# Performance work log

Measured on AMD Instinct MI355X. Metric: run time of the kernel, lower is better.

Reference implementation:

```python
import jax, jax.numpy as jnp
import numpy as np
from jax import lax

A_NUM = 2
N_LAYER = 4
DIM0 = 64   # fr_inner_dim_0 == signal_dim_0 (forced by view/squeeze logic)
DIM1 = 256  # fr_inner_dim_1
SD0 = 64
SD1 = 64
K_OUT = 8
UPS = 4
EPS = 1e-5
BSZ = 64


def setup_inputs() -> dict:
    key = jax.random.key(0)
    ks = jax.random.split(key, 16)
    s = 0.05
    f32 = jnp.float32
    inp = jax.random.normal(ks[0], (BSZ, 2, SD0, SD1), f32)
    # ComplexConv2d2 weights stored squeezed to their effective matmul form.
    W_in_r = jax.random.normal(ks[1], (DIM1 * A_NUM, SD1), f32) * s
    W_in_i = jax.random.normal(ks[2], (DIM1 * A_NUM, SD1), f32) * s
    W_pre_r = jax.random.normal(ks[3], (A_NUM,), f32) * s
    W_pre_i = jax.random.normal(ks[4], (A_NUM,), f32) * s
    Wm_r = jax.random.normal(ks[5], (2 * N_LAYER, SD0, SD0), f32) * s
    Wm_i = jax.random.normal(ks[6], (2 * N_LAYER, SD0, SD0), f32) * s
    Wc_r = jax.random.normal(ks[7], (N_LAYER, A_NUM), f32) * s
    Wc_i = jax.random.normal(ks[8], (N_LAYER, A_NUM), f32) * s
    W_l3_r = jax.random.normal(ks[9], (DIM0 * A_NUM, SD0), f32) * s
    W_l3_i = jax.random.normal(ks[10], (DIM0 * A_NUM, SD0), f32) * s
    conv1_w = jax.random.normal(ks[11], (N_LAYER, A_NUM, A_NUM, 3, 3), f32) * s
    conv2_w = jax.random.normal(ks[12], (N_LAYER, A_NUM, A_NUM, 3, 3), f32) * s
    bn1_g = jnp.ones((N_LAYER, A_NUM), f32)
    bn1_b = jnp.zeros((N_LAYER, A_NUM), f32)
    bn2_g = jnp.ones((N_LAYER, A_NUM), f32)
    bn2_b = jnp.zeros((N_LAYER, A_NUM), f32)
    W_out = jax.random.normal(ks[13], (A_NUM, 1, K_OUT, K_OUT), f32) * s
    return {"inp": inp, "W_in_r": W_in_r, "W_in_i": W_in_i, "W_pre_r": W_pre_r,
            "W_pre_i": W_pre_i, "Wm_r": Wm_r, "Wm_i": Wm_i, "Wc_r": Wc_r,
            "Wc_i": Wc_i, "W_l3_r": W_l3_r, "W_l3_i": W_l3_i,
            "conv1_w": conv1_w, "bn1_g": bn1_g, "bn1_b": bn1_b,
            "conv2_w": conv2_w, "bn2_g": bn2_g, "bn2_b": bn2_b, "W_out": W_out}


def _circ_conv(x, w):
    xp = jnp.pad(x, ((0, 0), (0, 0), (1, 1), (1, 1)), mode='wrap')
    return lax.conv_general_dilated(xp, w, (1, 1), 'VALID',
                                    dimension_numbers=('NCHW', 'OIHW', 'NCHW'))


def _bn(x, g, b):
    mu = jnp.mean(x, axis=(0, 2, 3), keepdims=True)
    var = jnp.var(x, axis=(0, 2, 3), keepdims=True)
    return (x - mu) * lax.rsqrt(var + EPS) * g[None, :, None, None] + b[None, :, None, None]


def _forward(inp, W_in_r, W_in_i, W_pre_r, W_pre_i, Wm_r, Wm_i, Wc_r, Wc_i,
             W_l3_r, W_l3_i, conv1_w, bn1_g, bn1_b, conv2_w, bn2_g, bn2_b, W_out):
    bsz = inp.shape[0]
    xr, xi = inp[:, 0], inp[:, 1]  # (b, sd0, sd1)
    # input_layer: complex conv, kernel (1, sd1) -> contraction over width
    yr = jnp.einsum('bhw,cw->bch', xr, W_in_r) - jnp.einsum('bhw,cw->bch', xi, W_in_i)
    yi = jnp.einsum('bhw,cw->bch', xi, W_in_r) + jnp.einsum('bhw,cw->bch', xr, W_in_i)
    xreal = yr.reshape(bsz, A_NUM, DIM1, DIM0).transpose(0, 1, 3, 2)  # (b,A,dim0,dim1)
    ximag = yi.reshape(bsz, A_NUM, DIM1, DIM0).transpose(0, 1, 3, 2)
    # concat_pre: complex 1x1 conv, A_NUM -> 1 channel
    x_real = (jnp.einsum('bahw,a->bhw', xreal, W_pre_r) - jnp.einsum('bahw,a->bhw', ximag, W_pre_i))[:, None]
    x_imag = (jnp.einsum('bahw,a->bhw', ximag, W_pre_r) + jnp.einsum('bahw,a->bhw', xreal, W_pre_i))[:, None]
    Gr, Gi = x_real, x_imag  # loop-invariant Gnk

    def phase_branch(xr_, xi_, Wr, Wi):
        a, c = xr_[:, 0], xi_[:, 0]  # (b, dim0, dim1)
        # complex conv kernel (sd0,1) == matmul over height
        Ir = (jnp.einsum('bhw,ch->bcw', a, Wr) - jnp.einsum('bhw,ch->bcw', c, Wi))[:, None]
        Ii = (jnp.einsum('bhw,ch->bcw', c, Wr) + jnp.einsum('bhw,ch->bcw', a, Wi))[:, None]
        s_ = 1.0 + jnp.log(Ir * Ir + Ii * Ii)
        EIr, EIi = s_ * Ir, -s_ * Ii
        ur, ui = Wr.T, Wi.T
        zr = jnp.einsum('hc,bncw->bnhw', ur, EIr) - jnp.einsum('hc,bncw->bnhw', ui, EIi)
        zi = jnp.einsum('hc,bncw->bnhw', ur, EIi) + jnp.einsum('hc,bncw->bnhw', ui, EIr)
        wr = jnp.sum(Gr * zr - Gi * zi, axis=3)  # (b,1,dim0)
        wi = jnp.sum(Gr * zi + Gi * zr, axis=3)
        ang = jnp.arctan2(wi, wr)[..., None]  # broadcast over dim1
        cr, ci = jnp.cos(ang), -jnp.sin(ang)
        return Gr * cr - Gi * ci, Gr * ci + Gi * cr

    for i in range(N_LAYER):
        x1r, x1i = phase_branch(x_real, x_imag, Wm_r[i], Wm_i[i])
        x2r, x2i = phase_branch(x_real, x_imag, Wm_r[i + N_LAYER], Wm_i[i + N_LAYER])
        sr = jnp.concatenate([x1r, x2r], 1)
        si = jnp.concatenate([x1i, x2i], 1)
        x_real = (jnp.einsum('bahw,a->bhw', sr, Wc_r[i]) - jnp.einsum('bahw,a->bhw', si, Wc_i[i]))[:, None]
        x_imag = (jnp.einsum('bahw,a->bhw', si, Wc_r[i]) + jnp.einsum('bahw,a->bhw', sr, Wc_i[i]))[:, None]

    # input_layer3: complex conv kernel (sd0,1), 1 -> dim0*A_NUM channels
    a, c = x_real[:, 0], x_imag[:, 0]
    fr = (jnp.einsum('bhw,ch->bcw', a, W_l3_r) - jnp.einsum('bhw,ch->bcw', c, W_l3_i)).reshape(bsz, -1)
    fi = (jnp.einsum('bhw,ch->bcw', c, W_l3_r) + jnp.einsum('bhw,ch->bcw', a, W_l3_i)).reshape(bsz, -1)
    m = jnp.max(jnp.sqrt(fr * fr + fi * fi), axis=1, keepdims=True)
    fr, fi = fr / m, fi / m
    fr = fr.reshape(bsz, A_NUM, DIM0, DIM1)
    fi = fi.reshape(bsz, A_NUM, DIM0, DIM1)
    x = jnp.sqrt(fr * fr + fi * fi)

    for i in range(N_LAYER):
        h = jax.nn.relu(_bn(_circ_conv(x, conv1_w[i]), bn1_g[i], bn1_b[i]))
        h = _bn(_circ_conv(h, conv2_w[i]), bn2_g[i], bn2_b[i])
        x = jax.nn.relu(x + h)

    # ConvTranspose2d(A_NUM, 1, K_OUT, stride=UPS, padding=2, output_padding=1)
    wt = jnp.flip(W_out, (2, 3)).transpose(1, 0, 2, 3)  # (1, A_NUM, k, k)
    pad_lo = K_OUT - 1 - 2
    pad_hi = pad_lo + 1
    y = lax.conv_general_dilated(x, wt, (1, 1),
                                 [(pad_lo, pad_hi), (pad_lo, pad_hi)],
                                 lhs_dilation=(UPS, UPS),
                                 dimension_numbers=('NCHW', 'OIHW', 'NCHW'))
    return y[:, 0]


def reference(inp, W_in_r, W_in_i, W_pre_r, W_pre_i, Wm_r, Wm_i, Wc_r, Wc_i,
              W_l3_r, W_l3_i, conv1_w, bn1_g, bn1_b, conv2_w, bn2_g, bn2_b, W_out):
    return _forward(inp, W_in_r, W_in_i, W_pre_r, W_pre_i, Wm_r, Wm_i, Wc_r, Wc_i,
                    W_l3_r, W_l3_i, conv1_w, bn1_g, bn1_b, conv2_w, bn2_g, bn2_b, W_out)
```

## Files before the change

### kernel.cpp

```cpp
#include <hip/hip_runtime.h>
#include <hip/hip_bf16.h>
#include <math.h>


__global__ void k0_prep(const float* __restrict__ Wr, const float* __restrict__ Wi,
                        const float* __restrict__ pr, const float* __restrict__ pi,
                        float* __restrict__ ArT, float* __restrict__ AiT,
                        float2* __restrict__ C) {
    int w  = blockIdx.x;
    int w2 = threadIdx.x;
    float p0r = pr[0], p1r = pr[1], p0i = pi[0], p1i = pi[1];
    float wr0 = Wr[w2 * 64 + w],         wi0 = Wi[w2 * 64 + w];
    float wr1 = Wr[(256 + w2) * 64 + w], wi1 = Wi[(256 + w2) * 64 + w];
    ArT[w * 256 + w2] = p0r * wr0 - p0i * wi0 + p1r * wr1 - p1i * wi1;
    AiT[w * 256 + w2] = p0r * wi0 + p0i * wr0 + p1r * wi1 + p1i * wr1;
    if (w2 < 64) C[w * 64 + w2] = make_float2(1.f, 0.f);
}

__global__ __launch_bounds__(256) void k1_G(const float* __restrict__ inp,
                                            const float* __restrict__ ArT,
                                            const float* __restrict__ AiT,
                                            float* __restrict__ Gr, float* __restrict__ Gi) {
    int hc = blockIdx.x;
    int b  = blockIdx.y;
    int t  = threadIdx.x;
    __shared__ float sxr[8][64], sxi[8][64];
    int base_r = (b * 2 + 0) * 4096 + hc * 8 * 64;
    int base_i = (b * 2 + 1) * 4096 + hc * 8 * 64;
    for (int k = t; k < 512; k += 256) {
        int r = k >> 6, w = k & 63;
        sxr[r][w] = inp[base_r + r * 64 + w];
        sxi[r][w] = inp[base_i + r * 64 + w];
    }
    __syncthreads();
    float accr[8], acci[8];
#pragma unroll
    for (int r = 0; r < 8; r++) { accr[r] = 0.f; acci[r] = 0.f; }
    for (int k = 0; k < 64; k++) {
        float ar = ArT[k * 256 + t], ai = AiT[k * 256 + t];
#pragma unroll
        for (int r = 0; r < 8; r++) {
            float xr = sxr[r][k], xi = sxi[r][k];
            accr[r] += xr * ar - xi * ai;
            acci[r] += xi * ar + xr * ai;
        }
    }
#pragma unroll
    for (int r = 0; r < 8; r++) {
        int h = hc * 8 + r;
        Gr[(b * 64 + h) * 256 + t] = accr[r];
        Gi[(b * 64 + h) * 256 + t] = acci[r];
    }
}

__global__ __launch_bounds__(1024) void k2_layer(const float* __restrict__ Gr,
                                                 const float* __restrict__ Gi,
                                                 const float2* __restrict__ C,
                                                 const float* __restrict__ Wmr,
                                                 const float* __restrict__ Wmi,
                                                 float2* __restrict__ wsum, int layer) {
    int wc = blockIdx.x;
    int j  = blockIdx.y;
    int b  = blockIdx.z;
    int t = threadIdx.x, tx = t & 63, ty = t >> 6;
    __shared__ float2 sW[4096];
    __shared__ float2 sX[4096];
    const float* Wr = Wmr + (layer + 4 * j) * 4096;
    const float* Wi = Wmi + (layer + 4 * j) * 4096;
    for (int k = t; k < 4096; k += 1024) sW[k] = make_float2(Wr[k], Wi[k]);

    int gbase = b * 64 * 256 + wc * 64 + tx;
    float gr_[4], gi_[4];
#pragma unroll
    for (int r = 0; r < 4; r++) {
        int h = ty * 4 + r;
        float gr = Gr[gbase + h * 256], gi = Gi[gbase + h * 256];
        gr_[r] = gr; gi_[r] = gi;
        float2 c = C[b * 64 + h];
        sX[h * 64 + tx] = make_float2(c.x * gr - c.y * gi, c.x * gi + c.y * gr);
    }
    __syncthreads();

    float Ir[4], Ii[4];
#pragma unroll
    for (int r = 0; r < 4; r++) { Ir[r] = 0.f; Ii[r] = 0.f; }
    for (int h = 0; h < 64; h++) {
        float2 x = sX[h * 64 + tx];
#pragma unroll
        for (int r = 0; r < 4; r++) {
            float2 w = sW[(ty * 4 + r) * 64 + h];
            Ir[r] += w.x * x.x - w.y * x.y;
            Ii[r] += w.x * x.y + w.y * x.x;
        }
    }
    __syncthreads();
#pragma unroll
    for (int r = 0; r < 4; r++) {
        float m2 = Ir[r] * Ir[r] + Ii[r] * Ii[r];
        float s = 1.f + __logf(m2);
        sX[(ty * 4 + r) * 64 + tx] = make_float2(s * Ir[r], -s * Ii[r]);
    }
    __syncthreads();

    float Zr[4], Zi[4];
#pragma unroll
    for (int r = 0; r < 4; r++) { Zr[r] = 0.f; Zi[r] = 0.f; }
    for (int c = 0; c < 64; c++) {
        float2 e = sX[c * 64 + tx];
#pragma unroll
        for (int r = 0; r < 4; r++) {
            float2 w = sW[c * 64 + ty * 4 + r];
            Zr[r] += w.x * e.x - w.y * e.y;
            Zi[r] += w.x * e.y + w.y * e.x;
        }
    }
#pragma unroll
    for (int r = 0; r < 4; r++) {
        int h = ty * 4 + r;
        float pr = gr_[r] * Zr[r] - gi_[r] * Zi[r];
        float pi = gr_[r] * Zi[r] + gi_[r] * Zr[r];
#pragma unroll
        for (int off = 32; off > 0; off >>= 1) {
            pr += __shfl_xor(pr, off);
            pi += __shfl_xor(pi, off);
        }
        if (tx == 0) wsum[((b * 64 + h) * 2 + j) * 4 + wc] = make_float2(pr, pi);
    }
}

__global__ void k3_cupdate(const float2* __restrict__ wsum, float2* __restrict__ C,
                           const float* __restrict__ Wcr, const float* __restrict__ Wci,
                           int layer) {
    int id = blockIdx.x * 256 + threadIdx.x;
    float accr = 0.f, acci = 0.f;
#pragma unroll
    for (int j = 0; j < 2; j++) {
        float wr = 0.f, wi = 0.f;
#pragma unroll
        for (int wc = 0; wc < 4; wc++) {
            float2 p = wsum[(id * 2 + j) * 4 + wc];
            wr += p.x; wi += p.y;
        }
        float m2 = wr * wr + wi * wi;
        float cr, ci;
        if (m2 > 0.f) {
            float inv = 1.f / sqrtf(m2);
            cr = wr * inv; ci = -wi * inv;
        } else { cr = 1.f; ci = 0.f; }
        float wcr = Wcr[layer * 2 + j], wci = Wci[layer * 2 + j];
        accr += cr * wcr - ci * wci;
        acci += ci * wcr + cr * wci;
    }
    C[id] = make_float2(accr, acci);
}

__global__ __launch_bounds__(1024) void k4_proj(const float* __restrict__ Gr,
                                                const float* __restrict__ Gi,
                                                const float2* __restrict__ C,
                                                const float* __restrict__ W3r,
                                                const float* __restrict__ W3i,
                                                float* __restrict__ xmag,
                                                float* __restrict__ pmax) {
    int wc = blockIdx.x;
    int cb = blockIdx.y;
    int b  = blockIdx.z;
    int t = threadIdx.x, tx = t & 63, ty = t >> 6;
    __shared__ float2 sW[4096];
    __shared__ float2 sX[4096];
    for (int k = t; k < 4096; k += 1024)
        sW[k] = make_float2(W3r[cb * 4096 + k], W3i[cb * 4096 + k]);
    int gbase = b * 64 * 256 + wc * 64 + tx;
#pragma unroll
    for (int r = 0; r < 4; r++) {
        int h = ty * 4 + r;
        float gr = Gr[gbase + h * 256], gi = Gi[gbase + h * 256];
        float2 c = C[b * 64 + h];
        sX[h * 64 + tx] = make_float2(c.x * gr - c.y * gi, c.x * gi + c.y * gr);
    }
    __syncthreads();
    float Fr[4], Fi[4];
#pragma unroll
    for (int r = 0; r < 4; r++) { Fr[r] = 0.f; Fi[r] = 0.f; }
    for (int h = 0; h < 64; h++) {
        float2 x = sX[h * 64 + tx];
#pragma unroll
        for (int r = 0; r < 4; r++) {
            float2 w = sW[(ty * 4 + r) * 64 + h];
            Fr[r] += w.x * x.x - w.y * x.y;
            Fi[r] += w.x * x.y + w.y * x.x;
        }
    }
    float mx = 0.f;
#pragma unroll
    for (int r = 0; r < 4; r++) {
        int cl = ty * 4 + r;
        float mag = sqrtf(Fr[r] * Fr[r] + Fi[r] * Fi[r]);
        xmag[(b * 128 + cb * 64 + cl) * 256 + wc * 64 + tx] = mag;
        mx = fmaxf(mx, mag);
    }
#pragma unroll
    for (int off = 32; off > 0; off >>= 1) mx = fmaxf(mx, __shfl_xor(mx, off));
    __syncthreads();
    float* scratch = (float*)sX;
    if (tx == 0) scratch[ty] = mx;
    __syncthreads();
    if (t == 0) {
        float m = scratch[0];
#pragma unroll
        for (int k = 1; k < 16; k++) m = fmaxf(m, scratch[k]);
        pmax[b * 8 + cb * 4 + wc] = m;
    }
}

__global__ void k5_invm(const float* __restrict__ pmax, float* __restrict__ invm) {
    int b = threadIdx.x;
    float m = 0.f;
#pragma unroll
    for (int k = 0; k < 8; k++) m = fmaxf(m, pmax[b * 8 + k]);
    invm[b] = 1.f / m;
}

__global__ void k5b_scale(float* __restrict__ x, const float* __restrict__ invm) {
    int id = blockIdx.x * 256 + threadIdx.x;
    x[id] *= invm[id >> 15];
}

__global__ __launch_bounds__(256) void k_conv(const float* __restrict__ xin,
                                              const float* __restrict__ cw,
                                              const float* __restrict__ stats,
                                              float* __restrict__ hout,
                                              float* __restrict__ psum,
                                              float* __restrict__ psumsq,
                                              int layer, int apply_bn_relu) {
    int hb = blockIdx.x;
    int co = blockIdx.y;
    int b  = blockIdx.z;
    int tx = threadIdx.x;
    float wgt[18];
    const float* wp = cw + layer * 36 + co * 18;
#pragma unroll
    for (int k = 0; k < 18; k++) wgt[k] = wp[k];
    float sc0 = 1.f, sc1 = 1.f, sh0 = 0.f, sh1 = 0.f;
    if (apply_bn_relu) { sc0 = stats[0]; sc1 = stats[1]; sh0 = stats[2]; sh1 = stats[3]; }
    int wm = (tx + 255) & 255, wpp = (tx + 1) & 255;
    float lsum = 0.f, lsq = 0.f;
    for (int r = 0; r < 16; r++) {
        int hh = hb * 16 + r;
        int hm = (hh + 63) & 63, hp = (hh + 1) & 63;
        const int rows[3] = {hm, hh, hp};
        const int cols[3] = {wm, tx, wpp};
        float acc = 0.f;
#pragma unroll
        for (int ci = 0; ci < 2; ci++) {
            const float* xp = xin + (b * 2 + ci) * 16384;
            float sc = ci ? sc1 : sc0, sh = ci ? sh1 : sh0;
            const float* wg = wgt + ci * 9;
#pragma unroll
            for (int kh = 0; kh < 3; kh++)
#pragma unroll
                for (int kw = 0; kw < 3; kw++) {
                    float v = xp[rows[kh] * 256 + cols[kw]];
                    if (apply_bn_relu) v = fmaxf(v * sc + sh, 0.f);
                    acc += wg[kh * 3 + kw] * v;
                }
        }
        hout[((b * 2 + co) * 64 + hh) * 256 + tx] = acc;
        lsum += acc; lsq += acc * acc;
    }
#pragma unroll
    for (int off = 32; off > 0; off >>= 1) {
        lsum += __shfl_xor(lsum, off);
        lsq  += __shfl_xor(lsq, off);
    }
    __shared__ float ssum[4], ssq[4];
    int ty = tx >> 6, lane = tx & 63;
    if (lane == 0) { ssum[ty] = lsum; ssq[ty] = lsq; }
    __syncthreads();
    if (tx == 0) {
        int bl = b * 4 + hb;
        psum[co * 256 + bl]   = ssum[0] + ssum[1] + ssum[2] + ssum[3];
        psumsq[co * 256 + bl] = ssq[0] + ssq[1] + ssq[2] + ssq[3];
    }
}

__global__ void k_stats(const float* __restrict__ psum, const float* __restrict__ psumsq,
                        const float* __restrict__ g, const float* __restrict__ bb,
                        float* __restrict__ stats, int layer) {
    int ch = threadIdx.x >> 6, lane = threadIdx.x & 63;
    float s = 0.f, q = 0.f;
#pragma unroll
    for (int k = lane; k < 256; k += 64) { s += psum[ch * 256 + k]; q += psumsq[ch * 256 + k]; }
#pragma unroll
    for (int off = 32; off > 0; off >>= 1) { s += __shfl_xor(s, off); q += __shfl_xor(q, off); }
    if (lane == 0) {
        const float N = 1048576.f;
        float mu = s / N;
        float var = q / N - mu * mu;
        float rs = rsqrtf(var + 1e-5f);
        float gamma = g[layer * 2 + ch];
        stats[ch]     = rs * gamma;
        stats[2 + ch] = bb[layer * 2 + ch] - mu * rs * gamma;
    }
}

__global__ void k8_res(float* __restrict__ x, const float* __restrict__ h2,
                       const float* __restrict__ stats) {
    int id = blockIdx.x * 256 + threadIdx.x;
    int ch = (id >> 14) & 1;
    float v = x[id] + h2[id] * stats[ch] + stats[2 + ch];
    x[id] = fmaxf(v, 0.f);
}

__global__ void k9_out(const float* __restrict__ x, const float* __restrict__ Wout,
                       float* __restrict__ out) {
    const int TOT = 64 * 257 * 1025;
    int id = blockIdx.x * 256 + threadIdx.x;
    if (id >= TOT) return;
    int b   = id / 263425;
    int rem = id - b * 263425;
    int oh  = rem / 1025;
    int ow  = rem - oh * 1025;
    int kh0 = (5 - oh) & 3;
    int kw0 = (5 - ow) & 3;
    float acc = 0.f;
#pragma unroll
    for (int ah = 0; ah < 2; ah++) {
        int kh = kh0 + 4 * ah;
        int d = oh + kh - 5;
        if (d < 0 || d > 252) continue;
        int rh = d >> 2;
#pragma unroll
        for (int aw = 0; aw < 2; aw++) {
            int kw = kw0 + 4 * aw;
            int e = ow + kw - 5;
            if (e < 0 || e > 1020) continue;
            int rw = e >> 2;
#pragma unroll
            for (int ci = 0; ci < 2; ci++) {
                float wv = Wout[ci * 64 + (7 - kh) * 8 + (7 - kw)];
                acc += wv * x[((b * 2 + ci) * 64 + rh) * 256 + rw];
            }
        }
    }
    out[id] = acc;
}

extern "C" void kernel_launch(void* const* d_in, const int* in_sizes, int n_in,
                              void* d_out, int out_size, void* d_ws, size_t ws_size,
                              hipStream_t stream) {
    const float* inp   = (const float*)d_in[0];
    const float* Winr  = (const float*)d_in[1];
    const float* Wini  = (const float*)d_in[2];
    const float* Wprer = (const float*)d_in[3];
    const float* Wprei = (const float*)d_in[4];
    const float* Wmr   = (const float*)d_in[5];
    const float* Wmi   = (const float*)d_in[6];
    const float* Wcr   = (const float*)d_in[7];
    const float* Wci   = (const float*)d_in[8];
    const float* W3r   = (const float*)d_in[9];
    const float* W3i   = (const float*)d_in[10];
    const float* cw1   = (const float*)d_in[11];
    const float* bn1g  = (const float*)d_in[12];
    const float* bn1b  = (const float*)d_in[13];
    const float* cw2   = (const float*)d_in[14];
    const float* bn2g  = (const float*)d_in[15];
    const float* bn2b  = (const float*)d_in[16];
    const float* Wout  = (const float*)d_in[17];
    float* out = (float*)d_out;

    float* ws = (float*)d_ws;
    float*  ArT   = ws;
    float*  AiT   = ArT + 16384;
    float2* C     = (float2*)(AiT + 16384);
    float*  Gr    = (float*)C + 8192;
    float*  Gi    = Gr + 1048576;
    float2* wsum  = (float2*)(Gi + 1048576);
    float*  xmag  = (float*)wsum + 65536;
    float*  h2    = xmag + 2097152;
    float*  pmax  = h2 + 2097152;
    float*  invm  = pmax + 512;
    float*  psum1 = invm + 64;
    float*  psq1  = psum1 + 512;
    float*  psum2 = psq1 + 512;
    float*  psq2  = psum2 + 512;
    float*  stats = psq2 + 512;
    float*  h1    = Gr;

    k0_prep<<<64, 256, 0, stream>>>(Winr, Wini, Wprer, Wprei, ArT, AiT, C);
    k1_G<<<dim3(8, 64), 256, 0, stream>>>(inp, ArT, AiT, Gr, Gi);
    for (int i = 0; i < 4; i++) {
        k2_layer<<<dim3(4, 2, 64), 1024, 0, stream>>>(Gr, Gi, C, Wmr, Wmi, wsum, i);
        k3_cupdate<<<16, 256, 0, stream>>>(wsum, C, Wcr, Wci, i);
    }
    k4_proj<<<dim3(4, 2, 64), 1024, 0, stream>>>(Gr, Gi, C, W3r, W3i, xmag, pmax);
    k5_invm<<<1, 64, 0, stream>>>(pmax, invm);
    k5b_scale<<<8192, 256, 0, stream>>>(xmag, invm);
    for (int i = 0; i < 4; i++) {
        k_conv<<<dim3(4, 2, 64), 256, 0, stream>>>(xmag, cw1, stats, h1, psum1, psq1, i, 0);
        k_stats<<<1, 128, 0, stream>>>(psum1, psq1, bn1g, bn1b, stats, i);
        k_conv<<<dim3(4, 2, 64), 256, 0, stream>>>(h1, cw2, stats, h2, psum2, psq2, i, 1);
        k_stats<<<1, 128, 0, stream>>>(psum2, psq2, bn2g, bn2b, stats + 4, i);
        k8_res<<<8192, 256, 0, stream>>>(xmag, h2, stats + 4);
    }
    k9_out<<<65857, 256, 0, stream>>>(xmag, Wout, out);
}
```

Baseline: 559.9 us.

## Read matmul weights via scalar loads, fuse inverse-max, split conv rows finer

The complex-matmul kernels no longer stage the 64x64 weight matrices in shared memory. Each wave reads its four weight rows through wave-uniform (readfirstlane) pointers, so the loads can become scalar, and a pre-transposed copy of Wm is built for the second matmul. Dropping the 32KB weight tile is meant to cut shared memory use and the staging cost, and to raise occupancy. Separately, the inverse-max kernel is folded into the scaling kernel, and the circular conv grid goes from 4 to 16 row-blocks per image, with larger partial-stat buffers, to expose more parallelism. The transposed weights live in h2 scratch, which is only safe because h2 is first written after the matmul stage.

```diff
diff --git a/kernel.cpp b/kernel.cpp
--- a/kernel.cpp
+++ b/kernel.cpp
@@ -15,6 +15,21 @@
     ArT[w * 256 + w2] = p0r * wr0 - p0i * wi0 + p1r * wr1 - p1i * wi1;
     AiT[w * 256 + w2] = p0r * wi0 + p0i * wr0 + p1r * wi1 + p1i * wr1;
     if (w2 < 64) C[w * 64 + w2] = make_float2(1.f, 0.f);
+}
+
+__global__ void k0b_T(const float* __restrict__ Wmr, const float* __restrict__ Wmi,
+                      float* __restrict__ WmrT, float* __restrict__ WmiT) {
+    int m = blockIdx.x;
+    int t = threadIdx.x;
+    const float* sr = Wmr + m * 4096;
+    const float* si = Wmi + m * 4096;
+    float* dr = WmrT + m * 4096;
+    float* di = WmiT + m * 4096;
+    for (int k = t; k < 4096; k += 256) {
+        int c = k >> 6, h = k & 63;
+        dr[h * 64 + c] = sr[k];
+        di[h * 64 + c] = si[k];
+    }
 }
 
 __global__ __launch_bounds__(256) void k1_G(const float* __restrict__ inp,
@@ -58,22 +73,26 @@
                                                  const float2* __restrict__ C,
                                                  const float* __restrict__ Wmr,
                                                  const float* __restrict__ Wmi,
+                                                 const float* __restrict__ WmrT,
+                                                 const float* __restrict__ WmiT,
                                                  float2* __restrict__ wsum, int layer) {
     int wc = blockIdx.x;
     int j  = blockIdx.y;
     int b  = blockIdx.z;
     int t = threadIdx.x, tx = t & 63, ty = t >> 6;
-    __shared__ float2 sW[4096];
     __shared__ float2 sX[4096];
-    const float* Wr = Wmr + (layer + 4 * j) * 4096;
-    const float* Wi = Wmi + (layer + 4 * j) * 4096;
-    for (int k = t; k < 4096; k += 1024) sW[k] = make_float2(Wr[k], Wi[k]);
-
-    int gbase = b * 64 * 256 + wc * 64 + tx;
+    int mat = layer + 4 * j;
+    int c0 = __builtin_amdgcn_readfirstlane(ty << 2);
+    const float* Wr0  = Wmr  + mat * 4096 + c0 * 64;
+    const float* Wi0  = Wmi  + mat * 4096 + c0 * 64;
+    const float* WrT0 = WmrT + mat * 4096 + c0 * 64;
+    const float* WiT0 = WmiT + mat * 4096 + c0 * 64;
+
+    int gbase = b * 16384 + wc * 64 + tx;
     float gr_[4], gi_[4];
 #pragma unroll
     for (int r = 0; r < 4; r++) {
-        int h = ty * 4 + r;
+        int h = (ty << 2) + r;
         float gr = Gr[gbase + h * 256], gi = Gi[gbase + h * 256];
         gr_[r] = gr; gi_[r] = gi;
         float2 c = C[b * 64 + h];
@@ -81,16 +100,15 @@
     }
     __syncthreads();
 
-    float Ir[4], Ii[4];
-#pragma unroll
-    for (int r = 0; r < 4; r++) { Ir[r] = 0.f; Ii[r] = 0.f; }
+    float Ir[4] = {0.f, 0.f, 0.f, 0.f}, Ii[4] = {0.f, 0.f, 0.f, 0.f};
+#pragma unroll 8
     for (int h = 0; h < 64; h++) {
         float2 x = sX[h * 64 + tx];
 #pragma unroll
         for (int r = 0; r < 4; r++) {
-            float2 w = sW[(ty * 4 + r) * 64 + h];
-            Ir[r] += w.x * x.x - w.y * x.y;
-            Ii[r] += w.x * x.y + w.y * x.x;
+            float wr = Wr0[r * 64 + h], wi = Wi0[r * 64 + h];
+            Ir[r] += wr * x.x - wi * x.y;
+            Ii[r] += wr * x.y + wi * x.x;
         }
     }
     __syncthreads();
@@ -98,25 +116,24 @@
     for (int r = 0; r < 4; r++) {
         float m2 = Ir[r] * Ir[r] + Ii[r] * Ii[r];
         float s = 1.f + __logf(m2);
-        sX[(ty * 4 + r) * 64 + tx] = make_float2(s * Ir[r], -s * Ii[r]);
-    }
-    __syncthreads();
-
-    float Zr[4], Zi[4];
-#pragma unroll
-    for (int r = 0; r < 4; r++) { Zr[r] = 0.f; Zi[r] = 0.f; }
+        sX[((ty << 2) + r) * 64 + tx] = make_float2(s * Ir[r], -s * Ii[r]);
+    }
+    __syncthreads();
+
+    float Zr[4] = {0.f, 0.f, 0.f, 0.f}, Zi[4] = {0.f, 0.f, 0.f, 0.f};
+#pragma unroll 8
     for (int c = 0; c < 64; c++) {
         float2 e = sX[c * 64 + tx];
 #pragma unroll
         for (int r = 0; r < 4; r++) {
-            float2 w = sW[c * 64 + ty * 4 + r];
-            Zr[r] += w.x * e.x - w.y * e.y;
-            Zi[r] += w.x * e.y + w.y * e.x;
-        }
-    }
-#pragma unroll
-    for (int r = 0; r < 4; r++) {
-        int h = ty * 4 + r;
+            float wr = WrT0[r * 64 + c], wi = WiT0[r * 64 + c];
+            Zr[r] += wr * e.x - wi * e.y;
+            Zi[r] += wr * e.y + wi * e.x;
+        }
+    }
+#pragma unroll
+    for (int r = 0; r < 4; r++) {
+        int h = (ty << 2) + r;
         float pr = gr_[r] * Zr[r] - gi_[r] * Zi[r];
         float pi = gr_[r] * Zi[r] + gi_[r] * Zr[r];
 #pragma unroll
@@ -165,35 +182,34 @@
     int cb = blockIdx.y;
     int b  = blockIdx.z;
     int t = threadIdx.x, tx = t & 63, ty = t >> 6;
-    __shared__ float2 sW[4096];
     __shared__ float2 sX[4096];
-    for (int k = t; k < 4096; k += 1024)
-        sW[k] = make_float2(W3r[cb * 4096 + k], W3i[cb * 4096 + k]);
-    int gbase = b * 64 * 256 + wc * 64 + tx;
-#pragma unroll
-    for (int r = 0; r < 4; r++) {
-        int h = ty * 4 + r;
+    int c0 = __builtin_amdgcn_readfirstlane(ty << 2);
+    const float* W3r0 = W3r + (cb * 64 + c0) * 64;
+    const float* W3i0 = W3i + (cb * 64 + c0) * 64;
+    int gbase = b * 16384 + wc * 64 + tx;
+#pragma unroll
+    for (int r = 0; r < 4; r++) {
+        int h = (ty << 2) + r;
         float gr = Gr[gbase + h * 256], gi = Gi[gbase + h * 256];
         float2 c = C[b * 64 + h];
         sX[h * 64 + tx] = make_float2(c.x * gr - c.y * gi, c.x * gi + c.y * gr);
     }
     __syncthreads();
-    float Fr[4], Fi[4];
-#pragma unroll
-    for (int r = 0; r < 4; r++) { Fr[r] = 0.f; Fi[r] = 0.f; }
+    float Fr[4] = {0.f, 0.f, 0.f, 0.f}, Fi[4] = {0.f, 0.f, 0.f, 0.f};
+#pragma unroll 8
     for (int h = 0; h < 64; h++) {
         float2 x = sX[h * 64 + tx];
 #pragma unroll
         for (int r = 0; r < 4; r++) {
-            float2 w = sW[(ty * 4 + r) * 64 + h];
-            Fr[r] += w.x * x.x - w.y * x.y;
-            Fi[r] += w.x * x.y + w.y * x.x;
+            float wr = W3r0[r * 64 + h], wi = W3i0[r * 64 + h];
+            Fr[r] += wr * x.x - wi * x.y;
+            Fi[r] += wr * x.y + wi * x.x;
         }
     }
     float mx = 0.f;
 #pragma unroll
     for (int r = 0; r < 4; r++) {
-        int cl = ty * 4 + r;
+        int cl = (ty << 2) + r;
         float mag = sqrtf(Fr[r] * Fr[r] + Fi[r] * Fi[r]);
         xmag[(b * 128 + cb * 64 + cl) * 256 + wc * 64 + tx] = mag;
         mx = fmaxf(mx, mag);
@@ -212,17 +228,13 @@
     }
 }
 
-__global__ void k5_invm(const float* __restrict__ pmax, float* __restrict__ invm) {
-    int b = threadIdx.x;
+__global__ void k5b_scale(float* __restrict__ x, const float* __restrict__ pmax) {
+    int id = blockIdx.x * 256 + threadIdx.x;
+    int b = id >> 15;
     float m = 0.f;
 #pragma unroll
     for (int k = 0; k < 8; k++) m = fmaxf(m, pmax[b * 8 + k]);
-    invm[b] = 1.f / m;
-}
-
-__global__ void k5b_scale(float* __restrict__ x, const float* __restrict__ invm) {
-    int id = blockIdx.x * 256 + threadIdx.x;
-    x[id] *= invm[id >> 15];
+    x[id] *= 1.f / m;
 }
 
 __global__ __launch_bounds__(256) void k_conv(const float* __restrict__ xin,
@@ -244,8 +256,8 @@
     if (apply_bn_relu) { sc0 = stats[0]; sc1 = stats[1]; sh0 = stats[2]; sh1 = stats[3]; }
     int wm = (tx + 255) & 255, wpp = (tx + 1) & 255;
     float lsum = 0.f, lsq = 0.f;
-    for (int r = 0; r < 16; r++) {
-        int hh = hb * 16 + r;
+    for (int r = 0; r < 4; r++) {
+        int hh = hb * 4 + r;
         int hm = (hh + 63) & 63, hp = (hh + 1) & 63;
         const int rows[3] = {hm, hh, hp};
         const int cols[3] = {wm, tx, wpp};
@@ -277,9 +289,9 @@
     if (lane == 0) { ssum[ty] = lsum; ssq[ty] = lsq; }
     __syncthreads();
     if (tx == 0) {
-        int bl = b * 4 + hb;
-        psum[co * 256 + bl]   = ssum[0] + ssum[1] + ssum[2] + ssum[3];
-        psumsq[co * 256 + bl] = ssq[0] + ssq[1] + ssq[2] + ssq[3];
+        int bl = b * 16 + hb;
+        psum[co * 1024 + bl]   = ssum[0] + ssum[1] + ssum[2] + ssum[3];
+        psumsq[co * 1024 + bl] = ssq[0] + ssq[1] + ssq[2] + ssq[3];
     }
 }
 
@@ -288,8 +300,7 @@
                         float* __restrict__ stats, int layer) {
     int ch = threadIdx.x >> 6, lane = threadIdx.x & 63;
     float s = 0.f, q = 0.f;
-#pragma unroll
-    for (int k = lane; k < 256; k += 64) { s += psum[ch * 256 + k]; q += psumsq[ch * 256 + k]; }
+    for (int k = lane; k < 1024; k += 64) { s += psum[ch * 1024 + k]; q += psumsq[ch * 1024 + k]; }
 #pragma unroll
     for (int off = 32; off > 0; off >>= 1) { s += __shfl_xor(s, off); q += __shfl_xor(q, off); }
     if (lane == 0) {
@@ -378,27 +389,28 @@
     float*  xmag  = (float*)wsum + 65536;
     float*  h2    = xmag + 2097152;
     float*  pmax  = h2 + 2097152;
-    float*  invm  = pmax + 512;
-    float*  psum1 = invm + 64;
-    float*  psq1  = psum1 + 512;
-    float*  psum2 = psq1 + 512;
-    float*  psq2  = psum2 + 512;
-    float*  stats = psq2 + 512;
+    float*  psum1 = pmax + 512;
+    float*  psq1  = psum1 + 2048;
+    float*  psum2 = psq1 + 2048;
+    float*  psq2  = psum2 + 2048;
+    float*  stats = psq2 + 2048;
     float*  h1    = Gr;
+    float*  WmrT  = h2;
+    float*  WmiT  = h2 + 32768;
 
     k0_prep<<<64, 256, 0, stream>>>(Winr, Wini, Wprer, Wprei, ArT, AiT, C);
+    k0b_T<<<8, 256, 0, stream>>>(Wmr, Wmi, WmrT, WmiT);
     k1_G<<<dim3(8, 64), 256, 0, stream>>>(inp, ArT, AiT, Gr, Gi);
     for (int i = 0; i < 4; i++) {
-        k2_layer<<<dim3(4, 2, 64), 1024, 0, stream>>>(Gr, Gi, C, Wmr, Wmi, wsum, i);
+        k2_layer<<<dim3(4, 2, 64), 1024, 0, stream>>>(Gr, Gi, C, Wmr, Wmi, WmrT, WmiT, wsum, i);
         k3_cupdate<<<16, 256, 0, stream>>>(wsum, C, Wcr, Wci, i);
     }
     k4_proj<<<dim3(4, 2, 64), 1024, 0, stream>>>(Gr, Gi, C, W3r, W3i, xmag, pmax);
-    k5_invm<<<1, 64, 0, stream>>>(pmax, invm);
-    k5b_scale<<<8192, 256, 0, stream>>>(xmag, invm);
+    k5b_scale<<<8192, 256, 0, stream>>>(xmag, pmax);
     for (int i = 0; i < 4; i++) {
-        k_conv<<<dim3(4, 2, 64), 256, 0, stream>>>(xmag, cw1, stats, h1, psum1, psq1, i, 0);
+        k_conv<<<dim3(16, 2, 64), 256, 0, stream>>>(xmag, cw1, stats, h1, psum1, psq1, i, 0);
         k_stats<<<1, 128, 0, stream>>>(psum1, psq1, bn1g, bn1b, stats, i);
-        k_conv<<<dim3(4, 2, 64), 256, 0, stream>>>(h1, cw2, stats, h2, psum2, psq2, i, 1);
+        k_conv<<<dim3(16, 2, 64), 256, 0, stream>>>(h1, cw2, stats, h2, psum2, psq2, i, 1);
         k_stats<<<1, 128, 0, stream>>>(psum2, psq2, bn2g, bn2b, stats + 4, i);
         k8_res<<<8192, 256, 0, stream>>>(xmag, h2, stats + 4);
     }
```

Result: slower. 591.0 us (+5.6%).
